# Kernel tuning notes

Measured on AMD Instinct MI355X. Metric: run time of the kernel, lower is better.

## Reference

```python
import jax, jax.numpy as jnp
import numpy as np


def setup_inputs() -> dict:
    key = jax.random.key(0)
    ks = jax.random.split(key, 8)
    B, C, P1, P2 = 8, 256, 2048, 4096
    Cq = C // 8
    return {
        "x1": jax.random.normal(ks[0], (B, C, P1), dtype=jnp.float32),
        "x2": jax.random.normal(ks[1], (B, C, P2), dtype=jnp.float32),
        "Wq": jax.random.normal(ks[2], (Cq, C), dtype=jnp.float32) * (1.0 / np.sqrt(C)),
        "bq": jnp.zeros((Cq,), dtype=jnp.float32),
        "Wk": jax.random.normal(ks[3], (Cq, C), dtype=jnp.float32) * (1.0 / np.sqrt(C)),
        "bk": jnp.zeros((Cq,), dtype=jnp.float32),
        "Wv": jax.random.normal(ks[4], (C, C), dtype=jnp.float32) * (1.0 / np.sqrt(C)),
        "bv": jnp.zeros((C,), dtype=jnp.float32),
        "alpha": jnp.ones((1,), dtype=jnp.float32),
    }


def reference(x1, x2, Wq, bq, Wk, bk, Wv, bv, alpha):
    # Conv1d(kernel_size=1) == pointwise linear over channel dim.
    # q: [B, P1, Cq]   (Q(x1) then permute(0,2,1))
    q = jnp.einsum('oc,bcp->bpo', Wq, x1) + bq[None, None, :]
    # k: [B, Cq, P2]
    k = jnp.einsum('oc,bcp->bop', Wk, x2) + bk[None, :, None]
    # v: [B, C, P1]
    v = jnp.einsum('oc,bcp->bop', Wv, x1) + bv[None, :, None]
    # energy: [B, P1, P2]; unscaled attention, softmax over P2
    energy = jnp.einsum('bpo,boq->bpq', q, k)
    attention = jax.nn.softmax(energy, axis=-1)
    # out: [B, C, P2]
    out = jnp.einsum('bcp,bpq->bcq', v, attention)
    return alpha * out + x2
```

## Files before the change

kernel.cpp:

```cpp
#include <hip/hip_runtime.h>

#define B 8
#define C 256
#define P1 2048
#define P2 4096
#define CQ 32

typedef _Float16 h8 __attribute__((ext_vector_type(8)));
typedef _Float16 h4 __attribute__((ext_vector_type(4)));
typedef float f4 __attribute__((ext_vector_type(4)));

#define MFMA16(a, b, c) __builtin_amdgcn_mfma_f32_16x16x32_f16(a, b, c, 0, 0, 0)

__global__ void prep_w(const float* __restrict__ Wq, const float* __restrict__ Wk,
                       const float* __restrict__ Wv,
                       _Float16* __restrict__ Wqh, _Float16* __restrict__ Wql,
                       _Float16* __restrict__ Wkh, _Float16* __restrict__ Wkl,
                       _Float16* __restrict__ Wvh) {
    const int i = blockIdx.x * 256 + threadIdx.x;
    if (i < CQ * C) {
        float a = Wq[i]; _Float16 h = (_Float16)a;
        Wqh[i] = h; Wql[i] = (_Float16)(a - (float)h);
        float b2 = Wk[i]; _Float16 h2 = (_Float16)b2;
        Wkh[i] = h2; Wkl[i] = (_Float16)(b2 - (float)h2);
    }
    for (int j = i; j < C * C; j += 32 * 256)
        Wvh[j] = (_Float16)Wv[j];
}

__global__ __launch_bounds__(256) void prep_qkv(
        const float* __restrict__ x1, const float* __restrict__ x2,
        const _Float16* __restrict__ Wqh, const _Float16* __restrict__ Wql,
        const _Float16* __restrict__ Wvh,
        const _Float16* __restrict__ Wkh, const _Float16* __restrict__ Wkl,
        const float* __restrict__ bq, const float* __restrict__ bv,
        const float* __restrict__ bk,
        _Float16* __restrict__ qhw, _Float16* __restrict__ qlw,
        _Float16* __restrict__ vhw,
        _Float16* __restrict__ khw, _Float16* __restrict__ klw) {
    __shared__ float xs[32][257];
    const int t = threadIdx.x;
    const int b = blockIdx.x;
    const int y = blockIdx.y;
    const bool is1 = (y < P1 / 32);
    const int p0 = (is1 ? y : y - P1 / 32) * 32;
    const float* xb = is1 ? x1 + (size_t)b * C * P1 : x2 + (size_t)b * C * P2;
    const int ps = is1 ? P1 : P2;

    {
        const int pl4 = t & 7, cb = t >> 3;
#pragma unroll
        for (int i = 0; i < 8; ++i) {
            const int c = cb + i * 32;
            f4 v = *(const f4*)&xb[(size_t)c * ps + p0 + pl4 * 4];
#pragma unroll
            for (int r = 0; r < 4; ++r) xs[pl4 * 4 + r][c] = v[r];
        }
    }
    __syncthreads();

    const int w = t >> 6, lane = t & 63, ln = lane & 15, quad = lane >> 4;
    const int nh = w & 1, ch = w >> 1;
    const int prow = nh * 16 + ln;

    if (is1) {
        f4 accv[8];
#pragma unroll
        for (int mt = 0; mt < 8; ++mt) accv[mt] = (f4){0.f, 0.f, 0.f, 0.f};
        f4 accq = {0.f, 0.f, 0.f, 0.f};

        for (int ks = 0; ks < 8; ++ks) {
            const int c0 = ks * 32 + quad * 8;
            h8 bh, bl;
#pragma unroll
            for (int j = 0; j < 8; ++j) {
                float xv = xs[prow][c0 + j];
                _Float16 hh = (_Float16)xv;
                bh[j] = hh; bl[j] = (_Float16)(xv - (float)hh);
            }
#pragma unroll
            for (int mt = 0; mt < 8; ++mt) {
                h8 a = *(const h8*)&Wvh[(size_t)((ch * 8 + mt) * 16 + ln) * C + c0];
                accv[mt] = MFMA16(a, bh, accv[mt]);
                accv[mt] = MFMA16(a, bl, accv[mt]);
            }
            {
                h8 aqh = *(const h8*)&Wqh[(size_t)(ch * 16 + ln) * C + c0];
                h8 aql = *(const h8*)&Wql[(size_t)(ch * 16 + ln) * C + c0];
                accq = MFMA16(aql, bh, accq);
                accq = MFMA16(aqh, bl, accq);
                accq = MFMA16(aqh, bh, accq);
            }
        }
#pragma unroll
        for (int mt = 0; mt < 8; ++mt) {
            int cb2 = (ch * 8 + mt) * 16 + quad * 4;
            f4 bvv = *(const f4*)&bv[cb2];
#pragma unroll
            for (int r = 0; r < 4; ++r)
                vhw[((size_t)b * C + cb2 + r) * P1 + p0 + prow] =
                    (_Float16)(accv[mt][r] + bvv[r]);
        }
        {
            int ob = ch * 16 + quad * 4;
            f4 bqv = *(const f4*)&bq[ob];
            h4 hv, lv;
#pragma unroll
            for (int r = 0; r < 4; ++r) {
                float val = accq[r] + bqv[r];
                _Float16 hh = (_Float16)val;
                hv[r] = hh; lv[r] = (_Float16)(val - (float)hh);
            }
            size_t row = ((size_t)b * P1 + p0 + prow) * CQ + ob;
            *(h4*)(qhw + row) = hv;
            *(h4*)(qlw + row) = lv;
        }
    } else {
        f4 accq = {0.f, 0.f, 0.f, 0.f};
        for (int ks = 0; ks < 8; ++ks) {
            const int c0 = ks * 32 + quad * 8;
            h8 bh, bl;
#pragma unroll
            for (int j = 0; j < 8; ++j) {
                float xv = xs[prow][c0 + j];
                _Float16 hh = (_Float16)xv;
                bh[j] = hh; bl[j] = (_Float16)(xv - (float)hh);
            }
            h8 akh = *(const h8*)&Wkh[(size_t)(ch * 16 + ln) * C + c0];
            h8 akl = *(const h8*)&Wkl[(size_t)(ch * 16 + ln) * C + c0];
            accq = MFMA16(akl, bh, accq);
            accq = MFMA16(akh, bl, accq);
            accq = MFMA16(akh, bh, accq);
        }
        {
            int ob = ch * 16 + quad * 4;
            f4 bkv = *(const f4*)&bk[ob];
            h4 hv, lv;
#pragma unroll
            for (int r = 0; r < 4; ++r) {
                float val = accq[r] + bkv[r];
                _Float16 hh = (_Float16)val;
                hv[r] = hh; lv[r] = (_Float16)(val - (float)hh);
            }
            size_t row = ((size_t)b * P2 + p0 + prow) * CQ + ob;
            *(h4*)(khw + row) = hv;
            *(h4*)(klw + row) = lv;
        }
    }
}

__global__ __launch_bounds__(512) void stats_l(
        const _Float16* __restrict__ qhi, const _Float16* __restrict__ qlo,
        const _Float16* __restrict__ khi, const _Float16* __restrict__ klo,
        float* __restrict__ linv) {
    __shared__ float lred[4][32];
    const int t = threadIdx.x;
    const int b = blockIdx.x;
    const int p0 = blockIdx.y * 32;
    const int w = t >> 6, lane = t & 63, ln = lane & 15, quad = lane >> 4;
    const int ptw = w & 1, qq = w >> 1;
    const int pbase = p0 + ptw * 16;

    h8 qh = *(const h8*)(qhi + ((size_t)b * P1 + pbase + ln) * CQ + quad * 8);
    h8 ql = *(const h8*)(qlo + ((size_t)b * P1 + pbase + ln) * CQ + quad * 8);

    const _Float16* khb = khi + (size_t)b * P2 * CQ;
    const _Float16* klb = klo + (size_t)b * P2 * CQ;
    const int base = qq * 1024;

    h8 kh0 = *(const h8*)(khb + (size_t)(base + ln) * CQ + quad * 8);
    h8 kl0 = *(const h8*)(klb + (size_t)(base + ln) * CQ + quad * 8);
    h8 kh1 = *(const h8*)(khb + (size_t)(base + 16 + ln) * CQ + quad * 8);
    h8 kl1 = *(const h8*)(klb + (size_t)(base + 16 + ln) * CQ + quad * 8);

    f4 acc = {0.f, 0.f, 0.f, 0.f};
    for (int ti = 0; ti < 64; ti += 2) {
        h8 ch0 = kh0, cl0 = kl0, ch1 = kh1, cl1 = kl1;
        if (ti + 2 < 64) {
            int q2 = base + (ti + 2) * 16 + ln;
            kh0 = *(const h8*)(khb + (size_t)q2 * CQ + quad * 8);
            kl0 = *(const h8*)(klb + (size_t)q2 * CQ + quad * 8);
            kh1 = *(const h8*)(khb + (size_t)(q2 + 16) * CQ + quad * 8);
            kl1 = *(const h8*)(klb + (size_t)(q2 + 16) * CQ + quad * 8);
        }
        f4 z = {0.f, 0.f, 0.f, 0.f};
        f4 e0 = MFMA16(ql, ch0, z);
        e0 = MFMA16(qh, cl0, e0);
        e0 = MFMA16(qh, ch0, e0);
        f4 e1 = MFMA16(ql, ch1, z);
        e1 = MFMA16(qh, cl1, e1);
        e1 = MFMA16(qh, ch1, e1);
#pragma unroll
        for (int r = 0; r < 4; ++r)
            acc[r] += __expf(e0[r]) + __expf(e1[r]);
    }
#pragma unroll
    for (int off = 1; off < 16; off <<= 1) {
#pragma unroll
        for (int r = 0; r < 4; ++r) acc[r] += __shfl_xor(acc[r], off);
    }
    if (ln == 0) *(f4*)&lred[qq][ptw * 16 + quad * 4] = acc;
    __syncthreads();
    if (t < 32)
        linv[(size_t)b * P1 + p0 + t] =
            1.0f / (lred[0][t] + lred[1][t] + lred[2][t] + lred[3][t]);
}

__global__ __launch_bounds__(512, 4) void attn_gemm(
        const _Float16* __restrict__ qhi, const _Float16* __restrict__ qlo,
        const _Float16* __restrict__ khi, const _Float16* __restrict__ klo,
        const _Float16* __restrict__ vhi, const float* __restrict__ linv,
        const float* __restrict__ x2, const float* __restrict__ alpha_p,
        float* __restrict__ out) {
    __shared__ _Float16 att_s[2][64][256];

    const int t  = threadIdx.x;
    const int b  = blockIdx.x & 7;
    const int q0 = (blockIdx.x >> 3) * 64;
    const int w  = t >> 6;
    const int lane = t & 63, ln = lane & 15, quad = lane >> 4;
    const int sw = ln & 7;

    h8 kh[4], kl[4];
#pragma unroll
    for (int nt = 0; nt < 4; ++nt) {
        int q = q0 + nt * 16 + ln;
        kh[nt] = *(const h8*)(khi + ((size_t)b * P2 + q) * CQ + quad * 8);
        kl[nt] = *(const h8*)(klo + ((size_t)b * P2 + q) * CQ + quad * 8);
    }

    f4 acc[2][4];
#pragma unroll
    for (int mt = 0; mt < 2; ++mt)
#pragma unroll
        for (int nt = 0; nt < 4; ++nt) acc[mt][nt] = (f4){0.f, 0.f, 0.f, 0.f};

    const _Float16* vrow0 = vhi + ((size_t)b * C + w * 32 + ln) * P1;
    const _Float16* vrow1 = vrow0 + (size_t)16 * P1;

    h8 nqh[2], nql[2];
#pragma unroll
    for (int pt = 0; pt < 2; ++pt) {
        size_t r = ((size_t)b * P1 + pt * 128 + w * 16 + ln) * CQ + quad * 8;
        nqh[pt] = *(const h8*)(qhi + r);
        nql[pt] = *(const h8*)(qlo + r);
    }

    for (int pc = 0; pc < P1 / 256; ++pc) {
        const int p0v = pc * 256;
        _Float16* abuf = &att_s[pc & 1][0][0];

#pragma unroll
        for (int pt = 0; pt < 2; ++pt) {
            h8 cqh = nqh[pt], cql = nql[pt];
            f4 lv = *(const f4*)(linv + (size_t)b * P1 + p0v + pt * 128
                                 + w * 16 + quad * 4);
            const int gb = (pt << 4) + (w << 1) + (quad >> 1);
            const int col = ((gb ^ sw) << 3) + ((quad & 1) << 2);
#pragma unroll
            for (int nt = 0; nt < 4; ++nt) {
                f4 z = {0.f, 0.f, 0.f, 0.f};
                f4 e = MFMA16(cql, kh[nt], z);
                e = MFMA16(cqh, kl[nt], e);
                e = MFMA16(cqh, kh[nt], e);
                h4 pk;
#pragma unroll
                for (int r = 0; r < 4; ++r)
                    pk[r] = (_Float16)(__expf(e[r]) * lv[r]);
                *(h4*)&abuf[(nt * 16 + ln) * 256 + col] = pk;
            }
        }
        __syncthreads();

        if (pc + 1 < P1 / 256) {
#pragma unroll
            for (int pt = 0; pt < 2; ++pt) {
                size_t r = ((size_t)b * P1 + p0v + 256 + pt * 128
                            + w * 16 + ln) * CQ + quad * 8;
                nqh[pt] = *(const h8*)(qhi + r);
                nql[pt] = *(const h8*)(qlo + r);
            }
        }

#pragma unroll
        for (int kk = 0; kk < 8; ++kk) {
            h8 bf[4];
#pragma unroll
            for (int nt = 0; nt < 4; ++nt) {
                int g = kk * 4 + quad;
                bf[nt] = *(const h8*)&abuf[(nt * 16 + ln) * 256 + ((g ^ sw) << 3)];
            }
            h8 av0 = *(const h8*)(vrow0 + p0v + kk * 32 + quad * 8);
            h8 av1 = *(const h8*)(vrow1 + p0v + kk * 32 + quad * 8);
            __builtin_amdgcn_s_setprio(1);
#pragma unroll
            for (int nt = 0; nt < 4; ++nt)
                acc[0][nt] = MFMA16(av0, bf[nt], acc[0][nt]);
#pragma unroll
            for (int nt = 0; nt < 4; ++nt)
                acc[1][nt] = MFMA16(av1, bf[nt], acc[1][nt]);
            __builtin_amdgcn_s_setprio(0);
        }
    }

    const float alpha = alpha_p[0];
#pragma unroll
    for (int mt = 0; mt < 2; ++mt) {
#pragma unroll
        for (int nt = 0; nt < 4; ++nt) {
            int q = q0 + nt * 16 + ln;
#pragma unroll
            for (int r = 0; r < 4; ++r) {
                int c = w * 32 + mt * 16 + quad * 4 + r;
                size_t o = ((size_t)b * C + c) * P2 + q;
                out[o] = fmaf(alpha, acc[mt][nt][r], x2[o]);
            }
        }
    }
}

extern "C" void kernel_launch(void* const* d_in, const int* in_sizes, int n_in,
                              void* d_out, int out_size, void* d_ws, size_t ws_size,
                              hipStream_t stream) {
    const float* x1    = (const float*)d_in[0];
    const float* x2    = (const float*)d_in[1];
    const float* Wq    = (const float*)d_in[2];
    const float* bq    = (const float*)d_in[3];
    const float* Wk    = (const float*)d_in[4];
    const float* bk    = (const float*)d_in[5];
    const float* Wv    = (const float*)d_in[6];
    const float* bv    = (const float*)d_in[7];
    const float* alpha = (const float*)d_in[8];
    float* out = (float*)d_out;

    _Float16* qh = (_Float16*)d_ws;
    _Float16* ql = qh + (size_t)B * P1 * CQ;
    _Float16* kh = ql + (size_t)B * P1 * CQ;
    _Float16* kl = kh + (size_t)B * P2 * CQ;
    _Float16* vh = kl + (size_t)B * P2 * CQ;
    _Float16* wqh = vh + (size_t)B * C * P1;
    _Float16* wql = wqh + CQ * C;
    _Float16* wkh = wql + CQ * C;
    _Float16* wkl = wkh + CQ * C;
    _Float16* wvh = wkl + CQ * C;
    float*    li  = (float*)(wvh + C * C);

    prep_w<<<dim3(32), 256, 0, stream>>>(Wq, Wk, Wv, wqh, wql, wkh, wkl, wvh);
    prep_qkv<<<dim3(B, P1 / 32 + P2 / 32), 256, 0, stream>>>(
        x1, x2, wqh, wql, wvh, wkh, wkl, bq, bv, bk, qh, ql, vh, kh, kl);
    stats_l<<<dim3(B, P1 / 32), 512, 0, stream>>>(qh, ql, kh, kl, li);
    attn_gemm<<<dim3(512), 512, 0, stream>>>(qh, ql, kh, kl, vh, li, x2, alpha, out);
}
```

Before: 246.2 us.

## Halve attention chunk size and reuse K fragments across two query tiles in stats

In the stats kernel each wave now handles both 16-row query tiles against a 512-column slice of K, so every K fragment it loads feeds two MFMA chains and the per-wave key range shrinks. In attn_gemm the P1 chunk drops from 256 to 128. Each wave computes one query tile per chunk, which halves the LDS attention buffer but doubles the number of loop iterations and __syncthreads barriers. The smaller LDS footprint may raise occupancy or reduce LDS pressure, at the cost of more synchronisation and less work per barrier.

Result: faster. 228.7 us (-7.1%).

```diff
diff --git a/kernel.cpp b/kernel.cpp
--- a/kernel.cpp
+++ b/kernel.cpp
@@ -153,30 +153,31 @@
         const _Float16* __restrict__ qhi, const _Float16* __restrict__ qlo,
         const _Float16* __restrict__ khi, const _Float16* __restrict__ klo,
         float* __restrict__ linv) {
-    __shared__ float lred[4][32];
+    __shared__ float lred[8][32];
     const int t = threadIdx.x;
     const int b = blockIdx.x;
     const int p0 = blockIdx.y * 32;
     const int w = t >> 6, lane = t & 63, ln = lane & 15, quad = lane >> 4;
-    const int ptw = w & 1, qq = w >> 1;
-    const int pbase = p0 + ptw * 16;
-
-    h8 qh = *(const h8*)(qhi + ((size_t)b * P1 + pbase + ln) * CQ + quad * 8);
-    h8 ql = *(const h8*)(qlo + ((size_t)b * P1 + pbase + ln) * CQ + quad * 8);
+
+    h8 qh0 = *(const h8*)(qhi + ((size_t)b * P1 + p0 + ln) * CQ + quad * 8);
+    h8 ql0 = *(const h8*)(qlo + ((size_t)b * P1 + p0 + ln) * CQ + quad * 8);
+    h8 qh1 = *(const h8*)(qhi + ((size_t)b * P1 + p0 + 16 + ln) * CQ + quad * 8);
+    h8 ql1 = *(const h8*)(qlo + ((size_t)b * P1 + p0 + 16 + ln) * CQ + quad * 8);
 
     const _Float16* khb = khi + (size_t)b * P2 * CQ;
     const _Float16* klb = klo + (size_t)b * P2 * CQ;
-    const int base = qq * 1024;
+    const int base = w * 512;
 
     h8 kh0 = *(const h8*)(khb + (size_t)(base + ln) * CQ + quad * 8);
     h8 kl0 = *(const h8*)(klb + (size_t)(base + ln) * CQ + quad * 8);
     h8 kh1 = *(const h8*)(khb + (size_t)(base + 16 + ln) * CQ + quad * 8);
     h8 kl1 = *(const h8*)(klb + (size_t)(base + 16 + ln) * CQ + quad * 8);
 
-    f4 acc = {0.f, 0.f, 0.f, 0.f};
-    for (int ti = 0; ti < 64; ti += 2) {
+    f4 acc0 = {0.f, 0.f, 0.f, 0.f};
+    f4 acc1 = {0.f, 0.f, 0.f, 0.f};
+    for (int ti = 0; ti < 32; ti += 2) {
         h8 ch0 = kh0, cl0 = kl0, ch1 = kh1, cl1 = kl1;
-        if (ti + 2 < 64) {
+        if (ti + 2 < 32) {
             int q2 = base + (ti + 2) * 16 + ln;
             kh0 = *(const h8*)(khb + (size_t)q2 * CQ + quad * 8);
             kl0 = *(const h8*)(klb + (size_t)q2 * CQ + quad * 8);
@@ -184,26 +185,43 @@
             kl1 = *(const h8*)(klb + (size_t)(q2 + 16) * CQ + quad * 8);
         }
         f4 z = {0.f, 0.f, 0.f, 0.f};
-        f4 e0 = MFMA16(ql, ch0, z);
-        e0 = MFMA16(qh, cl0, e0);
-        e0 = MFMA16(qh, ch0, e0);
-        f4 e1 = MFMA16(ql, ch1, z);
-        e1 = MFMA16(qh, cl1, e1);
-        e1 = MFMA16(qh, ch1, e1);
-#pragma unroll
-        for (int r = 0; r < 4; ++r)
-            acc[r] += __expf(e0[r]) + __expf(e1[r]);
+        f4 e0 = MFMA16(ql0, ch0, z);
+        e0 = MFMA16(qh0, cl0, e0);
+        e0 = MFMA16(qh0, ch0, e0);
+        f4 e1 = MFMA16(ql1, ch0, z);
+        e1 = MFMA16(qh1, cl0, e1);
+        e1 = MFMA16(qh1, ch0, e1);
+        f4 e2 = MFMA16(ql0, ch1, z);
+        e2 = MFMA16(qh0, cl1, e2);
+        e2 = MFMA16(qh0, ch1, e2);
+        f4 e3 = MFMA16(ql1, ch1, z);
+        e3 = MFMA16(qh1, cl1, e3);
+        e3 = MFMA16(qh1, ch1, e3);
+#pragma unroll
+        for (int r = 0; r < 4; ++r) {
+            acc0[r] += __expf(e0[r]) + __expf(e2[r]);
+            acc1[r] += __expf(e1[r]) + __expf(e3[r]);
+        }
     }
 #pragma unroll
     for (int off = 1; off < 16; off <<= 1) {
 #pragma unroll
-        for (int r = 0; r < 4; ++r) acc[r] += __shfl_xor(acc[r], off);
-    }
-    if (ln == 0) *(f4*)&lred[qq][ptw * 16 + quad * 4] = acc;
+        for (int r = 0; r < 4; ++r) {
+            acc0[r] += __shfl_xor(acc0[r], off);
+            acc1[r] += __shfl_xor(acc1[r], off);
+        }
+    }
+    if (ln == 0) {
+        *(f4*)&lred[w][quad * 4] = acc0;
+        *(f4*)&lred[w][16 + quad * 4] = acc1;
+    }
     __syncthreads();
-    if (t < 32)
-        linv[(size_t)b * P1 + p0 + t] =
-            1.0f / (lred[0][t] + lred[1][t] + lred[2][t] + lred[3][t]);
+    if (t < 32) {
+        float s = 0.f;
+#pragma unroll
+        for (int i = 0; i < 8; ++i) s += lred[i][t];
+        linv[(size_t)b * P1 + p0 + t] = 1.0f / s;
+    }
 }
 
 __global__ __launch_bounds__(512, 4) void attn_gemm(
@@ -212,7 +230,7 @@
         const _Float16* __restrict__ vhi, const float* __restrict__ linv,
         const float* __restrict__ x2, const float* __restrict__ alpha_p,
         float* __restrict__ out) {
-    __shared__ _Float16 att_s[2][64][256];
+    __shared__ _Float16 att_s[2][64][128];
 
     const int t  = threadIdx.x;
     const int b  = blockIdx.x & 7;
@@ -235,70 +253,62 @@
 #pragma unroll
         for (int nt = 0; nt < 4; ++nt) acc[mt][nt] = (f4){0.f, 0.f, 0.f, 0.f};
 
-    const _Float16* vrow0 = vhi + ((size_t)b * C + w * 32 + ln) * P1;
-    const _Float16* vrow1 = vrow0 + (size_t)16 * P1;
-
-    h8 nqh[2], nql[2];
-#pragma unroll
-    for (int pt = 0; pt < 2; ++pt) {
-        size_t r = ((size_t)b * P1 + pt * 128 + w * 16 + ln) * CQ + quad * 8;
-        nqh[pt] = *(const h8*)(qhi + r);
-        nql[pt] = *(const h8*)(qlo + r);
-    }
-
-    for (int pc = 0; pc < P1 / 256; ++pc) {
-        const int p0v = pc * 256;
+    h8 nqh, nql;
+    {
+        size_t r = ((size_t)b * P1 + w * 16 + ln) * CQ + quad * 8;
+        nqh = *(const h8*)(qhi + r);
+        nql = *(const h8*)(qlo + r);
+    }
+
+    const int wg   = w * 2 + (quad >> 1);
+    const int wcol = ((wg ^ sw) << 3) + (quad & 1) * 4;
+
+    for (int pc = 0; pc < P1 / 128; ++pc) {
+        const int p0v = pc * 128;
+        h8 cqh = nqh, cql = nql;
+        if (pc + 1 < P1 / 128) {
+            size_t r = ((size_t)b * P1 + p0v + 128 + w * 16 + ln) * CQ + quad * 8;
+            nqh = *(const h8*)(qhi + r);
+            nql = *(const h8*)(qlo + r);
+        }
+        f4 lv = *(const f4*)(linv + (size_t)b * P1 + p0v + w * 16 + quad * 4);
+
         _Float16* abuf = &att_s[pc & 1][0][0];
-
-#pragma unroll
-        for (int pt = 0; pt < 2; ++pt) {
-            h8 cqh = nqh[pt], cql = nql[pt];
-            f4 lv = *(const f4*)(linv + (size_t)b * P1 + p0v + pt * 128
-                                 + w * 16 + quad * 4);
-            const int gb = (pt << 4) + (w << 1) + (quad >> 1);
-            const int col = ((gb ^ sw) << 3) + ((quad & 1) << 2);
+#pragma unroll
+        for (int nt = 0; nt < 4; ++nt) {
+            f4 z = {0.f, 0.f, 0.f, 0.f};
+            f4 e = MFMA16(cql, kh[nt], z);
+            e = MFMA16(cqh, kl[nt], e);
+            e = MFMA16(cqh, kh[nt], e);
+            h4 pk;
+#pragma unroll
+            for (int r = 0; r < 4; ++r)
+                pk[r] = (_Float16)(__expf(e[r]) * lv[r]);
+            *(h4*)&abuf[(nt * 16 + ln) * 128 + wcol] = pk;
+        }
+        __syncthreads();
+
+#pragma unroll
+        for (int kk = 0; kk < 128; kk += 32) {
+            h8 bf[4];
 #pragma unroll
             for (int nt = 0; nt < 4; ++nt) {
-                f4 z = {0.f, 0.f, 0.f, 0.f};
-                f4 e = MFMA16(cql, kh[nt], z);
-                e = MFMA16(cqh, kl[nt], e);
-                e = MFMA16(cqh, kh[nt], e);
-                h4 pk;
-#pragma unroll
-                for (int r = 0; r < 4; ++r)
-                    pk[r] = (_Float16)(__expf(e[r]) * lv[r]);
-                *(h4*)&abuf[(nt * 16 + ln) * 256 + col] = pk;
-            }
-        }
-        __syncthreads();
-
-        if (pc + 1 < P1 / 256) {
-#pragma unroll
-            for (int pt = 0; pt < 2; ++pt) {
-                size_t r = ((size_t)b * P1 + p0v + 256 + pt * 128
-                            + w * 16 + ln) * CQ + quad * 8;
-                nqh[pt] = *(const h8*)(qhi + r);
-                nql[pt] = *(const h8*)(qlo + r);
-            }
-        }
-
-#pragma unroll
-        for (int kk = 0; kk < 8; ++kk) {
-            h8 bf[4];
-#pragma unroll
-            for (int nt = 0; nt < 4; ++nt) {
-                int g = kk * 4 + quad;
-                bf[nt] = *(const h8*)&abuf[(nt * 16 + ln) * 256 + ((g ^ sw) << 3)];
-            }
-            h8 av0 = *(const h8*)(vrow0 + p0v + kk * 32 + quad * 8);
-            h8 av1 = *(const h8*)(vrow1 + p0v + kk * 32 + quad * 8);
+                int bcol2 = (kk >> 3) + quad;
+                bf[nt] = *(const h8*)&abuf[(nt * 16 + ln) * 128 + ((bcol2 ^ sw) << 3)];
+            }
+            h8 av[2];
+#pragma unroll
+            for (int mt = 0; mt < 2; ++mt) {
+                size_t off = ((size_t)b * C + w * 32 + mt * 16 + ln) * P1
+                           + p0v + kk + quad * 8;
+                av[mt] = *(const h8*)(vhi + off);
+            }
             __builtin_amdgcn_s_setprio(1);
 #pragma unroll
-            for (int nt = 0; nt < 4; ++nt)
-                acc[0][nt] = MFMA16(av0, bf[nt], acc[0][nt]);
-#pragma unroll
-            for (int nt = 0; nt < 4; ++nt)
-                acc[1][nt] = MFMA16(av1, bf[nt], acc[1][nt]);
+            for (int mt = 0; mt < 2; ++mt)
+#pragma unroll
+                for (int nt = 0; nt < 4; ++nt)
+                    acc[mt][nt] = MFMA16(av[mt], bf[nt], acc[mt][nt]);
             __builtin_amdgcn_s_setprio(0);
         }
     }
```
